# Performance work log

Hardware: AMD Instinct MI355X
Metric: run time of the kernel (lower is better)

Reference implementation:

```python
import jax, jax.numpy as jnp
import numpy as np
import math

B, LQ, LK, D = 8, 4096, 32768, 64
LKS = min(8000, LK)                                    # sampled key window (K[:, :8000])
UPART = min(5 * LQ * int(np.ceil(np.log1p(LKS))), LKS)  # = 8000


def setup_inputs() -> dict:
    key = jax.random.key(0)
    k1, k2, k3, k4 = jax.random.split(key, 4)
    q = jax.random.normal(k1, (B, LQ, D), dtype=jnp.float32)
    K = jax.random.normal(k2, (B, LK, D), dtype=jnp.float32)
    V = jax.random.normal(k3, (B, LK, D), dtype=jnp.float32)
    index_sample = jax.random.randint(k4, (UPART,), 0, LKS)  # torch.randint(0, L_K, (U_part,))
    return {"q": q, "K": K, "V": V, "index_sample": index_sample}


def reference(q, K, V, index_sample):
    L_K = min(8000, K.shape[1])            # K_sample = K[:, :8000]; L_K = K_sample.size(1)
    L_Q = q.shape[1]
    d_k = q.shape[-1]
    log_L_Q = int(np.ceil(np.log1p(L_Q)))
    u = min(5 * log_L_Q, L_Q)

    # gather sampled keys (indices < 8000, indexing full K as in the source)
    K_samp = K[:, index_sample, :]                         # [B, U_part, D]
    QKs = jnp.einsum('bqd,bud->bqu', q, K_samp)            # [B, L_Q, U_part]
    # sparsity measure: max - mean (divided by L_K as in torch.div(sum, L_K))
    M = QKs.max(axis=-1) - QKs.sum(axis=-1) / L_K          # [B, L_Q]
    # torch topk(largest=False) -> smallest u values of M
    _, M_top = jax.lax.top_k(-M, u)                        # [B, u]
    Q_reduce = jnp.take_along_axis(q, M_top[:, :, None], axis=1)  # [B, u, D]

    attn_scores = jnp.einsum('bud,bkd->buk', Q_reduce, K) / math.sqrt(d_k)  # [B, u, L_K_full]
    attn_probs = jax.nn.softmax(attn_scores, axis=-1)
    attn_output = jnp.einsum('buk,bkd->bud', attn_probs, V)                  # [B, u, D]
    return attn_output, attn_scores
```

## Files before the change

kernel.cpp:

```cpp
#include <hip/hip_runtime.h>

#define BB 8
#define LQ 4096
#define LK 32768
#define DD 64
#define UU 8000
#define NU 45
#define TQ2 128
#define TUC 160
#define NCH (UU/TUC)
#define CHB (TUC*DD*2)
#define KT5 512
#define NT5 64

typedef short short8 __attribute__((ext_vector_type(8)));
typedef float floatx16 __attribute__((ext_vector_type(16)));

__device__ __forceinline__ float bf2f(unsigned short h){ return __uint_as_float(((unsigned int)h) << 16); }
__device__ __forceinline__ unsigned short f2bf(float f){
  unsigned int u = __float_as_uint(f);
  u += 0x7FFFu + ((u >> 16) & 1u);
  return (unsigned short)(u >> 16);
}
__device__ __forceinline__ unsigned int fkey(float v){
  unsigned int u = __float_as_uint(v);
  return (u & 0x80000000u) ? ~u : (u | 0x80000000u);
}

__global__ __launch_bounds__(256) void k_gather(const float* __restrict__ Kg, const int* __restrict__ idx,
                                                unsigned short* __restrict__ khi, unsigned short* __restrict__ kmid){
  const int b = blockIdx.y;
  const int row = blockIdx.x*32 + (threadIdx.x >> 3);
  const int oct = threadIdx.x & 7;
  const float* src = Kg + ((size_t)(b*LK + idx[row]))*DD + oct*8;
  float x[8];
  #pragma unroll
  for (int j=0;j<8;j++) x[j] = src[j];
  unsigned short h[8], m[8];
  #pragma unroll
  for (int j=0;j<8;j++){
    h[j] = f2bf(x[j]);
    m[j] = f2bf(x[j] - bf2f(h[j]));
  }
  const int osl = oct ^ (row & 7);
  size_t o = ((size_t)(b*UU + row))*DD + osl*8;
  #pragma unroll
  for (int j=0;j<8;j++){ khi[o+j]=h[j]; kmid[o+j]=m[j]; }
}

__global__ __launch_bounds__(64) void k_spart(const float* __restrict__ Kg, const int* __restrict__ idx,
                                              float* __restrict__ Spart){
  const int g = blockIdx.x, b = blockIdx.y, d = threadIdx.x;
  float acc = 0.0f;
  for (int j=0;j<64;j++){
    int u = g*64 + j;
    acc += Kg[((size_t)(b*LK + idx[u]))*DD + d];
  }
  Spart[((size_t)(b*125 + g))*DD + d] = acc;
}
__global__ __launch_bounds__(64) void k_sred(const float* __restrict__ Spart, float* __restrict__ Sb){
  const int b = blockIdx.x, d = threadIdx.x;
  float acc = 0.0f;
  for (int g=0; g<125; g++) acc += Spart[((size_t)(b*125 + g))*DD + d];
  Sb[b*DD + d] = acc;
}

__device__ __forceinline__ void stage_chunk(const char* gh, const char* gm,
                                            unsigned short* Bhb, unsigned short* Bmb,
                                            int w, int lane){
  #pragma unroll
  for (int i=0;i<5;i++){
    const int u = w*5 + i;
    if (u < 20){
      __builtin_amdgcn_global_load_lds(
        (const __attribute__((address_space(1))) void*)(gh + u*1024 + lane*16),
        (__attribute__((address_space(3))) void*)((char*)Bhb + u*1024 + lane*16),
        16, 0, 0);
    } else {
      __builtin_amdgcn_global_load_lds(
        (const __attribute__((address_space(1))) void*)(gm + (u-20)*1024 + lane*16),
        (__attribute__((address_space(3))) void*)((char*)Bmb + (u-20)*1024 + lane*16),
        16, 0, 0);
    }
  }
}

__global__ __launch_bounds__(512,2) void k_Mm(const float* __restrict__ q,
                                              const unsigned short* __restrict__ khi,
                                              const unsigned short* __restrict__ kmid,
                                              float* __restrict__ amaxG, int* __restrict__ acargG){
  const int wg = blockIdx.x;
  const int b = wg & 7, qt = wg >> 3;
  const int tid = threadIdx.x;
  const int w = tid >> 6, lane = tid & 63;
  const int tr = w & 3, sp = w >> 2;
  const int l31 = lane & 31, lh = lane >> 5;
  __shared__ __align__(16) unsigned short Bh[2][TUC*DD];
  __shared__ __align__(16) unsigned short Bm[2][TUC*DD];
  __shared__ float combV[TQ2][2];
  __shared__ int   combC[TQ2][2];

  const int qrow = qt*TQ2 + tr*32 + l31;
  short8 ahi[4], amid[4];
  {
    const float* qp = q + ((size_t)(b*LQ) + qrow)*DD;
    #pragma unroll
    for (int s=0;s<4;s++){
      const int d0 = s*16 + lh*8;
      float4 x0 = *(const float4*)(qp + d0);
      float4 x1 = *(const float4*)(qp + d0 + 4);
      float xs[8] = {x0.x,x0.y,x0.z,x0.w,x1.x,x1.y,x1.z,x1.w};
      short8 h, m;
      #pragma unroll
      for (int j=0;j<8;j++){
        unsigned short hb = f2bf(xs[j]);
        unsigned short mb = f2bf(xs[j] - bf2f(hb));
        h[j] = (short)hb; m[j] = (short)mb;
      }
      ahi[s]=h; amid[s]=m;
    }
  }

  float vmax[16]; int carg[16];
  #pragma unroll
  for (int r=0;r<16;r++){ vmax[r]=-INFINITY; carg[r]=0; }

  const size_t kbyte = (size_t)b*UU*DD*2;
  const char* ghbase = (const char*)khi + kbyte;
  const char* gmbase = (const char*)kmid + kbyte;

  stage_chunk(ghbase, gmbase, &Bh[0][0], &Bm[0][0], w, lane);
  int cur = 0;

  for (int c=0;c<NCH;c++){
    __syncthreads();
    if (c+1 < NCH){
      stage_chunk(ghbase + (size_t)(c+1)*CHB, gmbase + (size_t)(c+1)*CHB,
                  &Bh[cur^1][0], &Bm[cur^1][0], w, lane);
    }
    float lmax[16];
    #pragma unroll
    for (int r=0;r<16;r++) lmax[r] = -INFINITY;
    for (int t = ((c ^ sp) & 1); t < 5; t += 2){
      floatx16 accA = {0.f,0.f,0.f,0.f,0.f,0.f,0.f,0.f,0.f,0.f,0.f,0.f,0.f,0.f,0.f,0.f};
      floatx16 accB = {0.f,0.f,0.f,0.f,0.f,0.f,0.f,0.f,0.f,0.f,0.f,0.f,0.f,0.f,0.f,0.f};
      #pragma unroll
      for (int s=0;s<4;s++){
        const int eo = (t*32 + l31)*DD + (((s*2 + lh) ^ (l31 & 7))*8);
        short8 bh = *(const short8*)(&Bh[cur][eo]);
        short8 bm = *(const short8*)(&Bm[cur][eo]);
        if (s & 1){
          accB = __builtin_amdgcn_mfma_f32_32x32x16_bf16(amid[s], bh, accB, 0, 0, 0);
          accB = __builtin_amdgcn_mfma_f32_32x32x16_bf16(ahi[s],  bm, accB, 0, 0, 0);
          accB = __builtin_amdgcn_mfma_f32_32x32x16_bf16(ahi[s],  bh, accB, 0, 0, 0);
        } else {
          accA = __builtin_amdgcn_mfma_f32_32x32x16_bf16(amid[s], bh, accA, 0, 0, 0);
          accA = __builtin_amdgcn_mfma_f32_32x32x16_bf16(ahi[s],  bm, accA, 0, 0, 0);
          accA = __builtin_amdgcn_mfma_f32_32x32x16_bf16(ahi[s],  bh, accA, 0, 0, 0);
        }
      }
      #pragma unroll
      for (int r=0;r<16;r++) lmax[r] = fmaxf(lmax[r], accA[r] + accB[r]);
    }
    #pragma unroll
    for (int r=0;r<16;r++){
      if (lmax[r] > vmax[r]){ vmax[r] = lmax[r]; carg[r] = c; }
    }
    cur ^= 1;
  }
  #pragma unroll
  for (int st=1; st<32; st<<=1){
    #pragma unroll
    for (int r=0;r<16;r++){
      float ov = __shfl_xor(vmax[r], st);
      int   oc = __shfl_xor(carg[r], st);
      if (ov > vmax[r]){ vmax[r]=ov; carg[r]=oc; }
    }
  }
  if (l31 == 0){
    #pragma unroll
    for (int r=0;r<16;r++){
      int m = (r&3) + 8*(r>>2) + 4*lh;
      int ql = tr*32 + m;
      combV[ql][sp] = vmax[r];
      combC[ql][sp] = carg[r];
    }
  }
  __syncthreads();
  if (tid < TQ2){
    float v0 = combV[tid][0], v1 = combV[tid][1];
    int   c0 = combC[tid][0], c1 = combC[tid][1];
    bool t1 = v1 > v0;
    amaxG[(size_t)b*LQ + qt*TQ2 + tid] = t1 ? v1 : v0;
    acargG[(size_t)b*LQ + qt*TQ2 + tid] = t1 ? c1 : c0;
  }
}

__global__ __launch_bounds__(256) void k_bucket(const int* __restrict__ acargG,
                                                int* __restrict__ qlist, int* __restrict__ bstart){
  const int b = blockIdx.x, tid = threadIdx.x;
  __shared__ int cnt[NCH];
  __shared__ int pos[NCH];
  if (tid < NCH) cnt[tid] = 0;
  __syncthreads();
  for (int qq = tid; qq < LQ; qq += 256){
    int ch = acargG[(size_t)b*LQ + qq];
    ch = (ch < 0) ? 0 : ((ch >= NCH) ? NCH-1 : ch);
    atomicAdd(&cnt[ch], 1);
  }
  __syncthreads();
  if (tid == 0){
    int acc = 0;
    for (int c=0;c<NCH;c++){ pos[c] = acc; bstart[b*64 + c] = acc; acc += cnt[c]; }
    bstart[b*64 + NCH] = acc;
  }
  __syncthreads();
  for (int qq = tid; qq < LQ; qq += 256){
    int ch = acargG[(size_t)b*LQ + qq];
    ch = (ch < 0) ? 0 : ((ch >= NCH) ? NCH-1 : ch);
    int p = atomicAdd(&pos[ch], 1);
    p = (p < 0) ? 0 : ((p >= LQ) ? LQ-1 : p);
    qlist[(size_t)b*LQ + p] = qq;
  }
}

__global__ __launch_bounds__(256,3) void k_refb(const float* __restrict__ q, const float* __restrict__ Kg,
                                                const int* __restrict__ idx, const float* __restrict__ Sb,
                                                const int* __restrict__ qlist, const int* __restrict__ bstart,
                                                float* __restrict__ M){
  const int wg = blockIdx.x;
  const int b = wg & 7;
  const int r0 = wg >> 3;
  const int ch = r0 >> 1, half = r0 & 1;
  const int tid = threadIdx.x;
  const int w = tid >> 6, lane = tid & 63;
  const int quad = lane & 3, rg = lane >> 2;
  __shared__ __align__(16) float Kl[TUC*DD];
  float4* Kl4 = (float4*)Kl;
  for (int g = tid; g < TUC*16; g += 256){
    int row = g >> 4, s = g & 15;
    int gidx = idx[ch*TUC + row];
    float4 v = *(const float4*)(Kg + ((size_t)(b*LK + gidx))*DD + s*4);
    Kl4[row*16 + (s ^ (row & 7))] = v;
  }
  __syncthreads();

  const float4* sp4 = (const float4*)(Sb + b*DD + quad*16);
  const float4 S0 = sp4[0], S1 = sp4[1], S2 = sp4[2], S3 = sp4[3];
  const int sl0 = ((quad<<2)|0) ^ (rg & 7);
  const int sl1 = ((quad<<2)|1) ^ (rg & 7);
  const int sl2 = ((quad<<2)|2) ^ (rg & 7);
  const int sl3 = ((quad<<2)|3) ^ (rg & 7);
  const int rbs = rg*16;
  const int s0 = bstart[b*64 + ch], s1 = bstart[b*64 + ch + 1];
  const int gw = half*4 + w;

  for (int i = s0 + (gw<<1); i < s1; i += 16){
    const int qa = qlist[(size_t)b*LQ + i];
    const int i2 = (i+1 < s1) ? i+1 : i;
    const int qb = qlist[(size_t)b*LQ + i2];
    const float4* ap = (const float4*)(q + ((size_t)(b*LQ + qa))*DD + quad*16);
    const float4* bp = (const float4*)(q + ((size_t)(b*LQ + qb))*DD + quad*16);
    const float4 A0 = ap[0], A1 = ap[1], A2 = ap[2], A3 = ap[3];
    const float4 B0 = bp[0], B1 = bp[1], B2 = bp[2], B3 = bp[3];
    float mxa = -INFINITY, mxb = -INFINITY;
    #pragma unroll
    for (int p=0;p<10;p++){
      const int base = p*256 + rbs;
      float4 k0 = Kl4[base + sl0];
      float4 k1 = Kl4[base + sl1];
      float4 k2 = Kl4[base + sl2];
      float4 k3 = Kl4[base + sl3];
      float a0 = A0.x*k0.x, a1 = A0.y*k0.y, a2 = A0.z*k0.z, a3 = A0.w*k0.w;
      a0 = fmaf(A1.x,k1.x,a0); a1 = fmaf(A1.y,k1.y,a1); a2 = fmaf(A1.z,k1.z,a2); a3 = fmaf(A1.w,k1.w,a3);
      a0 = fmaf(A2.x,k2.x,a0); a1 = fmaf(A2.y,k2.y,a1); a2 = fmaf(A2.z,k2.z,a2); a3 = fmaf(A2.w,k2.w,a3);
      a0 = fmaf(A3.x,k3.x,a0); a1 = fmaf(A3.y,k3.y,a1); a2 = fmaf(A3.z,k3.z,a2); a3 = fmaf(A3.w,k3.w,a3);
      float c0 = B0.x*k0.x, c1 = B0.y*k0.y, c2 = B0.z*k0.z, c3 = B0.w*k0.w;
      c0 = fmaf(B1.x,k1.x,c0); c1 = fmaf(B1.y,k1.y,c1); c2 = fmaf(B1.z,k1.z,c2); c3 = fmaf(B1.w,k1.w,c3);
      c0 = fmaf(B2.x,k2.x,c0); c1 = fmaf(B2.y,k2.y,c1); c2 = fmaf(B2.z,k2.z,c2); c3 = fmaf(B2.w,k2.w,c3);
      c0 = fmaf(B3.x,k3.x,c0); c1 = fmaf(B3.y,k3.y,c1); c2 = fmaf(B3.z,k3.z,c2); c3 = fmaf(B3.w,k3.w,c3);
      float sa = (a0+a1)+(a2+a3);
      float sc = (c0+c1)+(c2+c3);
      sa += __shfl_xor(sa, 1);
      sa += __shfl_xor(sa, 2);
      sc += __shfl_xor(sc, 1);
      sc += __shfl_xor(sc, 2);
      mxa = fmaxf(mxa, sa);
      mxb = fmaxf(mxb, sc);
    }
    #pragma unroll
    for (int st=4; st<64; st<<=1){
      mxa = fmaxf(mxa, __shfl_xor(mxa, st));
      mxb = fmaxf(mxb, __shfl_xor(mxb, st));
    }
    float m0 = A0.x*S0.x, m1 = A0.y*S0.y, m2 = A0.z*S0.z, m3 = A0.w*S0.w;
    m0 = fmaf(A1.x,S1.x,m0); m1 = fmaf(A1.y,S1.y,m1); m2 = fmaf(A1.z,S1.z,m2); m3 = fmaf(A1.w,S1.w,m3);
    m0 = fmaf(A2.x,S2.x,m0); m1 = fmaf(A2.y,S2.y,m1); m2 = fmaf(A2.z,S2.z,m2); m3 = fmaf(A2.w,S2.w,m3);
    m0 = fmaf(A3.x,S3.x,m0); m1 = fmaf(A3.y,S3.y,m1); m2 = fmaf(A3.z,S3.z,m2); m3 = fmaf(A3.w,S3.w,m3);
    float msa = (m0+m1)+(m2+m3);
    msa += __shfl_xor(msa, 1);
    msa += __shfl_xor(msa, 2);
    float n0 = B0.x*S0.x, n1 = B0.y*S0.y, n2 = B0.z*S0.z, n3 = B0.w*S0.w;
    n0 = fmaf(B1.x,S1.x,n0); n1 = fmaf(B1.y,S1.y,n1); n2 = fmaf(B1.z,S1.z,n2); n3 = fmaf(B1.w,S1.w,n3);
    n0 = fmaf(B2.x,S2.x,n0); n1 = fmaf(B2.y,S2.y,n1); n2 = fmaf(B2.z,S2.z,n2); n3 = fmaf(B2.w,S2.w,n3);
    n0 = fmaf(B3.x,S3.x,n0); n1 = fmaf(B3.y,S3.y,n1); n2 = fmaf(B3.z,S3.z,n2); n3 = fmaf(B3.w,S3.w,n3);
    float msb = (n0+n1)+(n2+n3);
    msb += __shfl_xor(msb, 1);
    msb += __shfl_xor(msb, 2);
    if (lane == 0){
      M[(size_t)b*LQ + qa] = mxa - msa * (1.0f/8000.0f);
      if (i2 != i) M[(size_t)b*LQ + qb] = mxb - msb * (1.0f/8000.0f);
    }
  }
}

__global__ __launch_bounds__(256) void k_select(const float* __restrict__ Mg,
                                                const float* __restrict__ q,
                                                int* __restrict__ MtopG, float* __restrict__ Qred){
  const int b = blockIdx.x, tid = threadIdx.x;
  __shared__ float Mv[LQ];
  __shared__ unsigned long long wmin[4];
  __shared__ int mtop[NU];
  __shared__ int selB;
  for (int qq = tid; qq < LQ; qq += 256) Mv[qq] = Mg[(size_t)b*LQ + qq];
  __syncthreads();
  unsigned long long lm = ~0ull;
  #pragma unroll
  for (int i=0;i<16;i++){
    int qq = tid + 256*i;
    unsigned long long kk = (((unsigned long long)fkey(Mv[qq]))<<32) | (unsigned int)qq;
    lm = (kk < lm) ? kk : lm;
  }
  for (int i=0;i<NU;i++){
    unsigned long long v = lm;
    #pragma unroll
    for (int st=1; st<64; st<<=1){
      unsigned long long o = __shfl_xor(v, st);
      v = (o < v) ? o : v;
    }
    if ((tid & 63) == 0) wmin[tid>>6] = v;
    __syncthreads();
    if (tid == 0){
      unsigned long long g01 = (wmin[0] < wmin[1]) ? wmin[0] : wmin[1];
      unsigned long long g23 = (wmin[2] < wmin[3]) ? wmin[2] : wmin[3];
      unsigned long long g = (g01 < g23) ? g01 : g23;
      int sel = (int)(g & 0xFFFFFFFFull);
      mtop[i] = sel; selB = sel; Mv[sel] = INFINITY;
    }
    __syncthreads();
    int sel = selB;
    if (tid == (sel & 255)){
      unsigned long long nl = ~0ull;
      #pragma unroll
      for (int j=0;j<16;j++){
        int qq = tid + 256*j;
        unsigned long long kk = (((unsigned long long)fkey(Mv[qq]))<<32) | (unsigned int)qq;
        nl = (kk < nl) ? kk : nl;
      }
      lm = nl;
    }
    __syncthreads();
  }
  if (tid < NU) MtopG[b*NU + tid] = mtop[tid];
  for (int e = tid; e < NU*DD; e += 256){
    int ui = e >> 6, d = e & 63;
    Qred[((size_t)(b*NU + ui))*DD + d] = q[((size_t)(b*LQ + mtop[ui]))*DD + d];
  }
}

#define QFMA(i) { float4 p = qr4[i]; \
  a0 = fmaf(kv##i.x, p.x, a0); a1 = fmaf(kv##i.y, p.y, a1); \
  a2 = fmaf(kv##i.z, p.z, a2); a3 = fmaf(kv##i.w, p.w, a3); }

__global__ __launch_bounds__(256) void k_scores(const float* __restrict__ Kg,
                                                const float* __restrict__ Qred,
                                                float* __restrict__ out1){
  const int b = blockIdx.y;
  const int k = blockIdx.x*256 + threadIdx.x;
  const float4* kp4 = (const float4*)(Kg + ((size_t)(b*LK + k))*DD);
  const float4 kv0  = kp4[0],  kv1  = kp4[1],  kv2  = kp4[2],  kv3  = kp4[3];
  const float4 kv4  = kp4[4],  kv5  = kp4[5],  kv6  = kp4[6],  kv7  = kp4[7];
  const float4 kv8  = kp4[8],  kv9  = kp4[9],  kv10 = kp4[10], kv11 = kp4[11];
  const float4 kv12 = kp4[12], kv13 = kp4[13], kv14 = kp4[14], kv15 = kp4[15];
  for (int u=0; u<NU; u++){
    const float4* qr4 = (const float4*)(Qred + ((size_t)(b*NU+u))*DD);
    float a0 = 0.f, a1 = 0.f, a2 = 0.f, a3 = 0.f;
    QFMA(0)  QFMA(1)  QFMA(2)  QFMA(3)
    QFMA(4)  QFMA(5)  QFMA(6)  QFMA(7)
    QFMA(8)  QFMA(9)  QFMA(10) QFMA(11)
    QFMA(12) QFMA(13) QFMA(14) QFMA(15)
    float s = ((a0+a1)+(a2+a3)) * 0.125f;
    out1[((size_t)(b*NU+u)<<15) + k] = s;
  }
}

__global__ __launch_bounds__(256) void k_rowstats(const float* __restrict__ out1,
                                                  float* __restrict__ rowm, float* __restrict__ rowinvl){
  const int r = blockIdx.x, tid = threadIdx.x;
  const float* row = out1 + ((size_t)r << 15);
  __shared__ float red[256];
  float mx = -INFINITY;
  for (int k = tid; k < LK; k += 256) mx = fmaxf(mx, row[k]);
  red[tid] = mx; __syncthreads();
  for (int s=128;s>0;s>>=1){ if (tid<s) red[tid] = fmaxf(red[tid], red[tid+s]); __syncthreads(); }
  float m = red[0]; __syncthreads();
  float sm = 0.0f;
  for (int k = tid; k < LK; k += 256) sm += __expf(row[k] - m);
  red[tid] = sm; __syncthreads();
  for (int s=128;s>0;s>>=1){ if (tid<s) red[tid] += red[tid+s]; __syncthreads(); }
  if (tid==0){ rowm[r] = m; rowinvl[r] = 1.0f/red[0]; }
}

__global__ __launch_bounds__(512) void k_pv(const float* __restrict__ Vg,
                                            const float* __restrict__ out1,
                                            const float* __restrict__ rowm, const float* __restrict__ rowinvl,
                                            float* __restrict__ pvpart){
  const int kt = blockIdx.x, b = blockIdx.y, tid = threadIdx.x;
  const int lane = tid & 63, w = tid >> 6;
  const int u0 = w*6;
  __shared__ float Vl[128][65];
  __shared__ __align__(16) float Pl[48][132];
  float acc[6];
  #pragma unroll
  for (int j=0;j<6;j++) acc[j] = 0.0f;
  for (int sc=0; sc<4; sc++){
    const int k0 = kt*KT5 + sc*128;
    {
      int r = tid >> 2, h = tid & 3;
      const float* vp = Vg + ((size_t)(b*LK + k0 + r))*DD + h*16;
      #pragma unroll
      for (int j=0;j<4;j++){
        float4 t = ((const float4*)vp)[j];
        Vl[r][h*16 + 4*j]   = t.x;
        Vl[r][h*16 + 4*j+1] = t.y;
        Vl[r][h*16 + 4*j+2] = t.z;
        Vl[r][h*16 + 4*j+3] = t.w;
      }
    }
    for (int e = tid; e < 48*128; e += 512){
      int u = e >> 7, kk = e & 127;
      float p = 0.0f;
      if (u < NU){
        int r = b*NU + u;
        float s = out1[((size_t)r<<15) + k0 + kk];
        p = __expf(s - rowm[r]) * rowinvl[r];
      }
      Pl[u][kk] = p;
    }
    __syncthreads();
    for (int kk4=0; kk4<32; kk4++){
      float v0 = Vl[4*kk4+0][lane];
      float v1 = Vl[4*kk4+1][lane];
      float v2 = Vl[4*kk4+2][lane];
      float v3 = Vl[4*kk4+3][lane];
      #pragma unroll
      for (int j=0;j<6;j++){
        float4 p = *reinterpret_cast<const float4*>(&Pl[u0+j][4*kk4]);
        acc[j] = fmaf(p.w, v3, fmaf(p.z, v2, fmaf(p.y, v1, fmaf(p.x, v0, acc[j]))));
      }
    }
    __syncthreads();
  }
  #pragma unroll
  for (int j=0;j<6;j++){
    if (u0 + j < NU){
      pvpart[(((size_t)(b*NU + u0 + j))*NT5 + kt)*DD + lane] = acc[j];
    }
  }
}

__global__ __launch_bounds__(256) void k_final(const float* __restrict__ pvpart, float* __restrict__ out0){
  int e = blockIdx.x*256 + threadIdx.x;
  if (e >= BB*NU*DD) return;
  int d = e & 63; int r = e >> 6;
  float s = 0.0f;
  for (int t=0;t<NT5;t++) s += pvpart[((size_t)r*NT5 + t)*DD + d];
  out0[e] = s;
}

extern "C" void kernel_launch(void* const* d_in, const int* in_sizes, int n_in,
                              void* d_out, int out_size, void* d_ws, size_t ws_size,
                              hipStream_t stream){
  const float* q  = (const float*)d_in[0];
  const float* K  = (const float*)d_in[1];
  const float* V  = (const float*)d_in[2];
  const int* idx  = (const int*)d_in[3];
  float* out0 = (float*)d_out;
  float* out1 = out0 + BB*NU*DD;

  float* ws = (float*)d_ws;
  unsigned short* khi  = (unsigned short*)ws;
  float*  pvpart = ws;
  unsigned short* kmid = (unsigned short*)(ws + (size_t)BB*UU*DD/2);
  float* Spart   = ws + (size_t)BB*UU*DD;
  float* Sb      = Spart + 64000;
  float* amax    = Sb + 512;
  int*   acarg   = (int*)(amax + BB*LQ);
  float* Mbq     = (float*)(acarg + BB*LQ);
  float* Qred    = Mbq + BB*LQ;
  float* rowm    = Qred + (size_t)BB*NU*DD;
  float* rowinvl = rowm + 512;
  int*   Mtop    = (int*)(rowinvl + 512);
  int*   qlist   = Mtop + 512;
  int*   bstart  = qlist + (size_t)BB*LQ;

  k_gather<<<dim3(UU/32, BB), 256, 0, stream>>>(K, idx, khi, kmid);
  k_spart<<<dim3(125, BB), 64, 0, stream>>>(K, idx, Spart);
  k_sred<<<BB, 64, 0, stream>>>(Spart, Sb);
  k_Mm<<<(LQ/TQ2)*BB, 512, 0, stream>>>(q, khi, kmid, amax, acarg);
  k_bucket<<<BB, 256, 0, stream>>>(acarg, qlist, bstart);
  k_refb<<<NCH*2*BB, 256, 0, stream>>>(q, K, idx, Sb, qlist, bstart, Mbq);
  k_select<<<BB, 256, 0, stream>>>(Mbq, q, Mtop, Qred);
  k_scores<<<dim3(LK/256, BB), 256, 0, stream>>>(K, Qred, out1);
  k_rowstats<<<BB*NU, 256, 0, stream>>>(out1, rowm, rowinvl);
  k_pv<<<dim3(NT5, BB), 512, 0, stream>>>(V, out1, rowm, rowinvl, pvpart);
  k_final<<<(BB*NU*DD + 255)/256, 256, 0, stream>>>(pvpart, out0);
}
```

Before: 593.2 us.

## Give each wave two query row-tiles to reuse staged key fragments

Changes the k_Mm wave layout from 4 row-groups × 2 key splits to 2 row-groups × 4 key splits. Each wave now holds two 32-row query tiles and reuses every LDS-loaded key fragment for both. This halves LDS reads per MFMA and runs two independent accumulator chains. It costs more registers (doubled A fragments and max/argmax state) at launch bounds 512,2, which could cause spills. The 5 key tiles per chunk now divide unevenly over 4 splits, so one split gets two tiles, rotated across chunks to balance load.

```diff
diff --git a/kernel.cpp b/kernel.cpp
--- a/kernel.cpp
+++ b/kernel.cpp
@@ -93,16 +93,17 @@
   const int b = wg & 7, qt = wg >> 3;
   const int tid = threadIdx.x;
   const int w = tid >> 6, lane = tid & 63;
-  const int tr = w & 3, sp = w >> 2;
+  const int qg = w & 1, sp = w >> 1;
   const int l31 = lane & 31, lh = lane >> 5;
   __shared__ __align__(16) unsigned short Bh[2][TUC*DD];
   __shared__ __align__(16) unsigned short Bm[2][TUC*DD];
-  __shared__ float combV[TQ2][2];
-  __shared__ int   combC[TQ2][2];
-
-  const int qrow = qt*TQ2 + tr*32 + l31;
-  short8 ahi[4], amid[4];
-  {
+  __shared__ float combV[TQ2][4];
+  __shared__ int   combC[TQ2][4];
+
+  short8 ahi[2][4], amid[2][4];
+  #pragma unroll
+  for (int a=0;a<2;a++){
+    const int qrow = qt*TQ2 + qg*64 + a*32 + l31;
     const float* qp = q + ((size_t)(b*LQ) + qrow)*DD;
     #pragma unroll
     for (int s=0;s<4;s++){
@@ -117,13 +118,15 @@
         unsigned short mb = f2bf(xs[j] - bf2f(hb));
         h[j] = (short)hb; m[j] = (short)mb;
       }
-      ahi[s]=h; amid[s]=m;
-    }
-  }
-
-  float vmax[16]; int carg[16];
-  #pragma unroll
-  for (int r=0;r<16;r++){ vmax[r]=-INFINITY; carg[r]=0; }
+      ahi[a][s]=h; amid[a][s]=m;
+    }
+  }
+
+  float vmax[2][16]; int carg[2][16];
+  #pragma unroll
+  for (int a=0;a<2;a++)
+    #pragma unroll
+    for (int r=0;r<16;r++){ vmax[a][r]=-INFINITY; carg[a][r]=0; }
 
   const size_t kbyte = (size_t)b*UU*DD*2;
   const char* ghbase = (const char*)khi + kbyte;
@@ -138,61 +141,66 @@
       stage_chunk(ghbase + (size_t)(c+1)*CHB, gmbase + (size_t)(c+1)*CHB,
                   &Bh[cur^1][0], &Bm[cur^1][0], w, lane);
     }
-    float lmax[16];
-    #pragma unroll
-    for (int r=0;r<16;r++) lmax[r] = -INFINITY;
-    for (int t = ((c ^ sp) & 1); t < 5; t += 2){
-      floatx16 accA = {0.f,0.f,0.f,0.f,0.f,0.f,0.f,0.f,0.f,0.f,0.f,0.f,0.f,0.f,0.f,0.f};
-      floatx16 accB = {0.f,0.f,0.f,0.f,0.f,0.f,0.f,0.f,0.f,0.f,0.f,0.f,0.f,0.f,0.f,0.f};
+    const int tb = (sp + c) & 3;
+    #pragma unroll
+    for (int k=0;k<2;k++){
+      const int t = tb + k*4;
+      if (t < 5){
+        floatx16 acc0 = {0.f,0.f,0.f,0.f,0.f,0.f,0.f,0.f,0.f,0.f,0.f,0.f,0.f,0.f,0.f,0.f};
+        floatx16 acc1 = {0.f,0.f,0.f,0.f,0.f,0.f,0.f,0.f,0.f,0.f,0.f,0.f,0.f,0.f,0.f,0.f};
+        #pragma unroll
+        for (int s=0;s<4;s++){
+          const int eo = (t*32 + l31)*DD + (((s*2 + lh) ^ (l31 & 7))*8);
+          short8 bh = *(const short8*)(&Bh[cur][eo]);
+          short8 bm = *(const short8*)(&Bm[cur][eo]);
+          acc0 = __builtin_amdgcn_mfma_f32_32x32x16_bf16(amid[0][s], bh, acc0, 0, 0, 0);
+          acc0 = __builtin_amdgcn_mfma_f32_32x32x16_bf16(ahi[0][s],  bm, acc0, 0, 0, 0);
+          acc0 = __builtin_amdgcn_mfma_f32_32x32x16_bf16(ahi[0][s],  bh, acc0, 0, 0, 0);
+          acc1 = __builtin_amdgcn_mfma_f32_32x32x16_bf16(amid[1][s], bh, acc1, 0, 0, 0);
+          acc1 = __builtin_amdgcn_mfma_f32_32x32x16_bf16(ahi[1][s],  bm, acc1, 0, 0, 0);
+          acc1 = __builtin_amdgcn_mfma_f32_32x32x16_bf16(ahi[1][s],  bh, acc1, 0, 0, 0);
+        }
+        #pragma unroll
+        for (int r=0;r<16;r++){
+          if (acc0[r] > vmax[0][r]){ vmax[0][r] = acc0[r]; carg[0][r] = c; }
+          if (acc1[r] > vmax[1][r]){ vmax[1][r] = acc1[r]; carg[1][r] = c; }
+        }
+      }
+    }
+    cur ^= 1;
+  }
+  #pragma unroll
+  for (int st=1; st<32; st<<=1){
+    #pragma unroll
+    for (int a=0;a<2;a++)
       #pragma unroll
-      for (int s=0;s<4;s++){
-        const int eo = (t*32 + l31)*DD + (((s*2 + lh) ^ (l31 & 7))*8);
-        short8 bh = *(const short8*)(&Bh[cur][eo]);
-        short8 bm = *(const short8*)(&Bm[cur][eo]);
-        if (s & 1){
-          accB = __builtin_amdgcn_mfma_f32_32x32x16_bf16(amid[s], bh, accB, 0, 0, 0);
-          accB = __builtin_amdgcn_mfma_f32_32x32x16_bf16(ahi[s],  bm, accB, 0, 0, 0);
-          accB = __builtin_amdgcn_mfma_f32_32x32x16_bf16(ahi[s],  bh, accB, 0, 0, 0);
-        } else {
-          accA = __builtin_amdgcn_mfma_f32_32x32x16_bf16(amid[s], bh, accA, 0, 0, 0);
-          accA = __builtin_amdgcn_mfma_f32_32x32x16_bf16(ahi[s],  bm, accA, 0, 0, 0);
-          accA = __builtin_amdgcn_mfma_f32_32x32x16_bf16(ahi[s],  bh, accA, 0, 0, 0);
-        }
-      }
+      for (int r=0;r<16;r++){
+        float ov = __shfl_xor(vmax[a][r], st);
+        int   oc = __shfl_xor(carg[a][r], st);
+        if (ov > vmax[a][r]){ vmax[a][r]=ov; carg[a][r]=oc; }
+      }
+  }
+  if (l31 == 0){
+    #pragma unroll
+    for (int a=0;a<2;a++)
       #pragma unroll
-      for (int r=0;r<16;r++) lmax[r] = fmaxf(lmax[r], accA[r] + accB[r]);
-    }
-    #pragma unroll
-    for (int r=0;r<16;r++){
-      if (lmax[r] > vmax[r]){ vmax[r] = lmax[r]; carg[r] = c; }
-    }
-    cur ^= 1;
-  }
-  #pragma unroll
-  for (int st=1; st<32; st<<=1){
-    #pragma unroll
-    for (int r=0;r<16;r++){
-      float ov = __shfl_xor(vmax[r], st);
-      int   oc = __shfl_xor(carg[r], st);
-      if (ov > vmax[r]){ vmax[r]=ov; carg[r]=oc; }
-    }
-  }
-  if (l31 == 0){
-    #pragma unroll
-    for (int r=0;r<16;r++){
-      int m = (r&3) + 8*(r>>2) + 4*lh;
-      int ql = tr*32 + m;
-      combV[ql][sp] = vmax[r];
-      combC[ql][sp] = carg[r];
-    }
+      for (int r=0;r<16;r++){
+        int m = (r&3) + 8*(r>>2) + 4*lh;
+        int ql = qg*64 + a*32 + m;
+        combV[ql][sp] = vmax[a][r];
+        combC[ql][sp] = carg[a][r];
+      }
   }
   __syncthreads();
   if (tid < TQ2){
-    float v0 = combV[tid][0], v1 = combV[tid][1];
-    int   c0 = combC[tid][0], c1 = combC[tid][1];
-    bool t1 = v1 > v0;
-    amaxG[(size_t)b*LQ + qt*TQ2 + tid] = t1 ? v1 : v0;
-    acargG[(size_t)b*LQ + qt*TQ2 + tid] = t1 ? c1 : c0;
+    float bv = combV[tid][0]; int bc = combC[tid][0];
+    #pragma unroll
+    for (int s=1;s<4;s++){
+      float v = combV[tid][s];
+      if (v > bv){ bv = v; bc = combC[tid][s]; }
+    }
+    amaxG[(size_t)b*LQ + qt*TQ2 + tid] = bv;
+    acargG[(size_t)b*LQ + qt*TQ2 + tid] = bc;
   }
 }
 
```

Measured after the change: 609.7 us. 1.03x slower.

## Fuse softmax row statistics into score kernel; split refinement across more workgroups

Applied to the files above, without the earlier changes.

The score kernel now computes a per-wavefront max and sum of exponentials for each score row and writes these partials. A small reduction kernel then combines them online-softmax style, replacing the pass that re-read the full 45x32768 score matrix per batch. Separately, the refinement kernel splits each chunk's query list across four workgroups instead of two, which adds parallelism at the cost of reloading the K tile into shared memory more often. The fused reductions add shuffle work inside the score loop.

```diff
diff --git a/kernel.cpp b/kernel.cpp
--- a/kernel.cpp
+++ b/kernel.cpp
@@ -231,7 +231,7 @@
   const int wg = blockIdx.x;
   const int b = wg & 7;
   const int r0 = wg >> 3;
-  const int ch = r0 >> 1, half = r0 & 1;
+  const int ch = r0 >> 2, part = r0 & 3;
   const int tid = threadIdx.x;
   const int w = tid >> 6, lane = tid & 63;
   const int quad = lane & 3, rg = lane >> 2;
@@ -253,9 +253,9 @@
   const int sl3 = ((quad<<2)|3) ^ (rg & 7);
   const int rbs = rg*16;
   const int s0 = bstart[b*64 + ch], s1 = bstart[b*64 + ch + 1];
-  const int gw = half*4 + w;
-
-  for (int i = s0 + (gw<<1); i < s1; i += 16){
+  const int gw = part*4 + w;
+
+  for (int i = s0 + (gw<<1); i < s1; i += 32){
     const int qa = qlist[(size_t)b*LQ + i];
     const int i2 = (i+1 < s1) ? i+1 : i;
     const int qb = qlist[(size_t)b*LQ + i2];
@@ -374,9 +374,12 @@
 
 __global__ __launch_bounds__(256) void k_scores(const float* __restrict__ Kg,
                                                 const float* __restrict__ Qred,
-                                                float* __restrict__ out1){
+                                                float* __restrict__ out1,
+                                                float* __restrict__ pm, float* __restrict__ pl){
   const int b = blockIdx.y;
   const int k = blockIdx.x*256 + threadIdx.x;
+  const int lane = threadIdx.x & 63, w = threadIdx.x >> 6;
+  const int pi = blockIdx.x*4 + w;
   const float4* kp4 = (const float4*)(Kg + ((size_t)(b*LK + k))*DD);
   const float4 kv0  = kp4[0],  kv1  = kp4[1],  kv2  = kp4[2],  kv3  = kp4[3];
   const float4 kv4  = kp4[4],  kv5  = kp4[5],  kv6  = kp4[6],  kv7  = kp4[7];
@@ -391,21 +394,32 @@
     QFMA(12) QFMA(13) QFMA(14) QFMA(15)
     float s = ((a0+a1)+(a2+a3)) * 0.125f;
     out1[((size_t)(b*NU+u)<<15) + k] = s;
-  }
-}
-
-__global__ __launch_bounds__(256) void k_rowstats(const float* __restrict__ out1,
-                                                  float* __restrict__ rowm, float* __restrict__ rowinvl){
+    float mw = s;
+    #pragma unroll
+    for (int st=1; st<64; st<<=1) mw = fmaxf(mw, __shfl_xor(mw, st));
+    float e = __expf(s - mw);
+    #pragma unroll
+    for (int st=1; st<64; st<<=1) e += __shfl_xor(e, st);
+    if (lane == 0){
+      size_t r = (size_t)(b*NU + u);
+      pm[r*512 + pi] = mw;
+      pl[r*512 + pi] = e;
+    }
+  }
+}
+
+__global__ __launch_bounds__(256) void k_rowred(const float* __restrict__ pm, const float* __restrict__ pl,
+                                                float* __restrict__ rowm, float* __restrict__ rowinvl){
   const int r = blockIdx.x, tid = threadIdx.x;
-  const float* row = out1 + ((size_t)r << 15);
   __shared__ float red[256];
-  float mx = -INFINITY;
-  for (int k = tid; k < LK; k += 256) mx = fmaxf(mx, row[k]);
-  red[tid] = mx; __syncthreads();
+  float m = -INFINITY;
+  for (int i = tid; i < 512; i += 256) m = fmaxf(m, pm[(size_t)r*512 + i]);
+  red[tid] = m; __syncthreads();
   for (int s=128;s>0;s>>=1){ if (tid<s) red[tid] = fmaxf(red[tid], red[tid+s]); __syncthreads(); }
-  float m = red[0]; __syncthreads();
+  m = red[0]; __syncthreads();
   float sm = 0.0f;
-  for (int k = tid; k < LK; k += 256) sm += __expf(row[k] - m);
+  for (int i = tid; i < 512; i += 256)
+    sm += pl[(size_t)r*512 + i] * __expf(pm[(size_t)r*512 + i] - m);
   red[tid] = sm; __syncthreads();
   for (int s=128;s>0;s>>=1){ if (tid<s) red[tid] += red[tid+s]; __syncthreads(); }
   if (tid==0){ rowm[r] = m; rowinvl[r] = 1.0f/red[0]; }
@@ -492,6 +506,8 @@
   unsigned short* khi  = (unsigned short*)ws;
   float*  pvpart = ws;
   unsigned short* kmid = (unsigned short*)(ws + (size_t)BB*UU*DD/2);
+  float* pm      = ws + (size_t)BB*UU*DD/2;
+  float* pl      = pm + (size_t)BB*NU*512;
   float* Spart   = ws + (size_t)BB*UU*DD;
   float* Sb      = Spart + 64000;
   float* amax    = Sb + 512;
@@ -509,10 +525,10 @@
   k_sred<<<BB, 64, 0, stream>>>(Spart, Sb);
   k_Mm<<<(LQ/TQ2)*BB, 512, 0, stream>>>(q, khi, kmid, amax, acarg);
   k_bucket<<<BB, 256, 0, stream>>>(acarg, qlist, bstart);
-  k_refb<<<NCH*2*BB, 256, 0, stream>>>(q, K, idx, Sb, qlist, bstart, Mbq);
+  k_refb<<<NCH*4*BB, 256, 0, stream>>>(q, K, idx, Sb, qlist, bstart, Mbq);
   k_select<<<BB, 256, 0, stream>>>(Mbq, q, Mtop, Qred);
-  k_scores<<<dim3(LK/256, BB), 256, 0, stream>>>(K, Qred, out1);
-  k_rowstats<<<BB*NU, 256, 0, stream>>>(out1, rowm, rowinvl);
+  k_scores<<<dim3(LK/256, BB), 256, 0, stream>>>(K, Qred, out1, pm, pl);
+  k_rowred<<<BB*NU, 256, 0, stream>>>(pm, pl, rowm, rowinvl);
   k_pv<<<dim3(NT5, BB), 512, 0, stream>>>(V, out1, rowm, rowinvl, pvpart);
   k_final<<<(BB*NU*DD + 255)/256, 256, 0, stream>>>(pvpart, out0);
 }
```

After: 523.5 us. 11.8% less time.
